# Optimization experiments

Measured on AMD Instinct MI355X. Metric: run time of the kernel, lower is better.

Reference implementation:

```python
import jax, jax.numpy as jnp
import numpy as np

B, N, K = 8, 2048, 32
EPS = 1e-5


def _lrelu(x):
    return jnp.where(x >= 0, x, 0.2 * x)


def _bn(x, p):
    # inference BatchNorm; x: [B, C, ...], p: [4, C] = (gamma, beta, mean, var)
    g, b, m, v = p[0], p[1], p[2], p[3]
    shape = (1, -1) + (1,) * (x.ndim - 2)
    scale = g * jax.lax.rsqrt(v + EPS)
    return (x - m.reshape(shape)) * scale.reshape(shape) + b.reshape(shape)


def _group(x, k):
    # ops.group with xyz_or_feature='feature', feature_or_diff='diff'
    # x: [B, C, N] -> edge features [B, 2C, N, k] = cat(neighbor - center, center)
    xt = jnp.transpose(x, (0, 2, 1))  # [B, N, C]
    sq = jnp.sum(xt * xt, axis=-1)    # [B, N]
    dist = sq[:, :, None] - 2.0 * jnp.einsum('bnc,bmc->bnm', xt, xt) + sq[:, None, :]
    idx = jax.lax.top_k(-dist, k)[1]  # [B, N, k] nearest neighbors
    nbr = jax.vmap(lambda f, i: f[i])(xt, idx)  # [B, N, k, C]
    center = xt[:, :, None, :]
    edge = jnp.concatenate([nbr - center, jnp.broadcast_to(center, nbr.shape)], axis=-1)
    return jnp.transpose(edge, (0, 3, 1, 2))  # [B, 2C, N, k]


def _edgeconv(x, w1, bn1, w2, bn2, k):
    e = _group(x, k)
    h = _lrelu(_bn(jnp.einsum('oc,bcnk->bonk', w1, e), bn1))
    h = _lrelu(_bn(jnp.einsum('oc,bcnk->bonk', w2, h), bn2))
    return jnp.max(h, axis=-1)  # max over neighbors -> [B, C_out, N]


def _model(x,
           ec1_w1, ec1_bn1, ec1_w2, ec1_bn2,
           ec2_w1, ec2_bn1, ec2_w2, ec2_bn2,
           ec3_w1, ec3_bn1, ec3_w2, ec3_bn2,
           emb_w, q_w, k_w, v_w, att_bn1, ff_w1, ff_w2, att_bn2,
           cb_w, cb_bn):
    # EdgeConvBlock (3 stacked EdgeConvs, outputs concatenated)
    f1 = _edgeconv(x, ec1_w1, ec1_bn1, ec1_w2, ec1_bn2, K)
    f2 = _edgeconv(f1, ec2_w1, ec2_bn1, ec2_w2, ec2_bn2, K)
    f3 = _edgeconv(f2, ec3_w1, ec3_bn1, ec3_w2, ec3_bn2, K)
    xc = jnp.concatenate([f1, f2, f3], axis=1)  # [B, 192, N]
    # Point2PointAttentionBlock: embedding then dense self-attention
    h = jnp.einsum('oc,bcn->bon', emb_w, xc)  # [B, 1024, N]
    q = jnp.einsum('oc,bcn->bon', q_w, h)
    kk = jnp.einsum('oc,bcn->bon', k_w, h)
    v = jnp.einsum('oc,bcn->bon', v_w, h)
    scale = jnp.sqrt(jnp.asarray(h.shape[1], h.dtype))
    att = jax.nn.softmax(jnp.einsum('bcn,bcm->bnm', q, kk) / scale, axis=-1)  # [B, N, N]
    x_r = jnp.einsum('bnm,bcm->bcn', att, v)
    h = _bn(h + x_r, att_bn1)
    ff = jnp.einsum('oc,bcn->bon', ff_w2, _lrelu(jnp.einsum('oc,bcn->bon', ff_w1, h)))
    h = _bn(h + ff, att_bn2)
    # ConvBlock head
    return _lrelu(_bn(jnp.einsum('oc,bcn->bon', cb_w, h), cb_bn))  # [B, 1024, N]


def setup_inputs() -> dict:
    key = jax.random.key(0)
    ks = iter(jax.random.split(key, 32))

    def randn(shape, s=0.1):
        return jax.random.normal(next(ks), shape, jnp.float32) * s

    def bnp(c):
        return jax.random.uniform(next(ks), (4, c), jnp.float32, 0.1, 1.0)

    return {
        'x': randn((B, 3, N), 1.0),
        'ec1_w1': randn((64, 6)), 'ec1_bn1': bnp(64),
        'ec1_w2': randn((64, 64)), 'ec1_bn2': bnp(64),
        'ec2_w1': randn((64, 128)), 'ec2_bn1': bnp(64),
        'ec2_w2': randn((64, 64)), 'ec2_bn2': bnp(64),
        'ec3_w1': randn((64, 128)), 'ec3_bn1': bnp(64),
        'ec3_w2': randn((64, 64)), 'ec3_bn2': bnp(64),
        'emb_w': randn((1024, 192), 0.05),
        'q_w': randn((1024, 1024), 0.03),
        'k_w': randn((1024, 1024), 0.03),
        'v_w': randn((1024, 1024), 0.03),
        'att_bn1': bnp(1024),
        'ff_w1': randn((512, 1024), 0.03),
        'ff_w2': randn((1024, 512), 0.03),
        'att_bn2': bnp(1024),
        'cb_w': randn((1024, 1024), 0.03),
        'cb_bn': bnp(1024),
    }


def reference(x,
              ec1_w1, ec1_bn1, ec1_w2, ec1_bn2,
              ec2_w1, ec2_bn1, ec2_w2, ec2_bn2,
              ec3_w1, ec3_bn1, ec3_w2, ec3_bn2,
              emb_w, q_w, k_w, v_w, att_bn1, ff_w1, ff_w2, att_bn2,
              cb_w, cb_bn):
    return _model(x,
                  ec1_w1, ec1_bn1, ec1_w2, ec1_bn2,
                  ec2_w1, ec2_bn1, ec2_w2, ec2_bn2,
                  ec3_w1, ec3_bn1, ec3_w2, ec3_bn2,
                  emb_w, q_w, k_w, v_w, att_bn1, ff_w1, ff_w2, att_bn2,
                  cb_w, cb_bn)
```

## Files before the change

### kernel.cpp

```cpp
#include <hip/hip_runtime.h>
#include <hip/hip_bf16.h>

constexpr int Bn  = 8;
constexpr int Np  = 2048;
constexpr int KNN = 32;

typedef __attribute__((ext_vector_type(8))) short bf16x8;
typedef __attribute__((ext_vector_type(4))) float f32x4;

__device__ static inline void gll16(const void* g, void* l) {
  __builtin_amdgcn_global_load_lds((const __attribute__((address_space(1))) void*)g,
                                   (__attribute__((address_space(3))) void*)l, 16, 0, 0);
}

__device__ static inline unsigned short f2bf(float x) {
  union { __hip_bfloat16 h; unsigned short u; } cv; cv.h = __float2bfloat16(x); return cv.u;
}
__device__ static inline float bf2f(unsigned short u) {
  union { __hip_bfloat16 h; unsigned short u; } cv; cv.u = u; return __bfloat162float(cv.h);
}

__global__ __launch_bounds__(256)
void cvt_bf16_kernel(const float* __restrict__ s, __hip_bfloat16* __restrict__ d, int n) {
  int i = blockIdx.x * 256 + threadIdx.x;
  if (i < n) d[i] = __float2bfloat16(s[i]);
}

template<int CIN, int K1>
__global__ __launch_bounds__(256)
void cvt_w1a(const float* __restrict__ w1, __hip_bfloat16* __restrict__ out) {
  int i = blockIdx.x * 256 + threadIdx.x;
  if (i >= 64 * K1) return;
  int o = i / K1, c = i - o * K1;
  out[i] = __float2bfloat16(c < CIN ? w1[o * 2 * CIN + c] : 0.f);
}

__global__ __launch_bounds__(256)
void xpose_kernel(const float* __restrict__ x, float* __restrict__ xt,
                  __hip_bfloat16* __restrict__ xb) {
  int i = blockIdx.x * 256 + threadIdx.x;
  int b = i >> 11, n = i & 2047;
  const float* p = x + (long)b * 3 * Np + n;
  float vx = p[0], vy = p[Np], vz = p[2 * Np];
  xt[(long)i * 4 + 0] = vx;
  xt[(long)i * 4 + 1] = vy;
  xt[(long)i * 4 + 2] = vz;
  xt[(long)i * 4 + 3] = 0.f;
  __hip_bfloat16* q = xb + (long)i * 8;
  q[0] = __float2bfloat16(vx); q[1] = __float2bfloat16(vy);
  q[2] = __float2bfloat16(vz);
  q[3] = __float2bfloat16(0.f); q[4] = q[3]; q[5] = q[3]; q[6] = q[3]; q[7] = q[3];
}

template<int C, int CP>
__global__ __launch_bounds__(256)
void sq_kernel(const float* __restrict__ f, float* __restrict__ out) {
  int i = blockIdx.x * 256 + threadIdx.x;
  const float* p = f + (long)i * CP;
  float s = 0.f;
#pragma unroll
  for (int c = 0; c < C; ++c) s += p[c] * p[c];
  out[i] = s;
}

__global__ __launch_bounds__(256)
void dist_kernel(const float* __restrict__ A, int lda, long sA,
                 float* __restrict__ C, long sC,
                 const float* __restrict__ sqB, int Kd) {
  int bz = blockIdx.z;
  A += (long)bz * sA;
  C += (long)bz * sC;
  sqB += (long)bz * Np;
  int i0 = blockIdx.y * 128, j0 = blockIdx.x * 128;
  __shared__ float As[8][128];
  __shared__ float Bs[8][128];
  float acc[8][8];
#pragma unroll
  for (int a = 0; a < 8; ++a)
#pragma unroll
    for (int b2 = 0; b2 < 8; ++b2) acc[a][b2] = 0.f;
  int t = threadIdx.x;
  int tx = t & 15, ty = t >> 4;
  for (int k0 = 0; k0 < Kd; k0 += 8) {
    {
      int ii = t >> 1, kk = (t & 1) * 4;
#pragma unroll
      for (int u = 0; u < 4; ++u) {
        int kg = k0 + kk + u;
        As[kk + u][ii] = (kg < Kd) ? A[(long)(i0 + ii) * lda + kg] : 0.f;
        Bs[kk + u][ii] = (kg < Kd) ? A[(long)(j0 + ii) * lda + kg] : 0.f;
      }
    }
    __syncthreads();
#pragma unroll
    for (int kk = 0; kk < 8; ++kk) {
      float av[8], bv[8];
#pragma unroll
      for (int u = 0; u < 8; ++u) av[u] = As[kk][ty * 8 + u];
#pragma unroll
      for (int u = 0; u < 8; ++u) bv[u] = Bs[kk][tx * 8 + u];
#pragma unroll
      for (int a = 0; a < 8; ++a)
#pragma unroll
        for (int b2 = 0; b2 < 8; ++b2) acc[a][b2] += av[a] * bv[b2];
    }
    __syncthreads();
  }
#pragma unroll
  for (int a = 0; a < 8; ++a) {
    int i = i0 + ty * 8 + a;
#pragma unroll
    for (int b2 = 0; b2 < 8; ++b2) {
      int j = j0 + tx * 8 + b2;
      C[(long)i * Np + j] = sqB[j] - 2.f * acc[a][b2];
    }
  }
}


__device__ static inline unsigned umin32(unsigned a, unsigned b) { return a < b ? a : b; }

__device__ static inline unsigned long long shfl64x(unsigned long long k, int m) {
  unsigned lo = (unsigned)__shfl_xor((int)(unsigned)k, m);
  unsigned hi = (unsigned)__shfl_xor((int)(unsigned)(k >> 32), m);
  return ((unsigned long long)hi << 32) | (unsigned long long)lo;
}

__device__ static inline unsigned lane_sort64_u32(unsigned v, int lane) {
#pragma unroll
  for (int k = 2; k <= 64; k <<= 1) {
#pragma unroll
    for (int j = k >> 1; j > 0; j >>= 1) {
      unsigned o = (unsigned)__shfl_xor((int)v, j);
      bool dir = ((lane & k) == 0);
      bool lower = ((lane & j) == 0);
      bool keep = (v < o) == (dir == lower);
      v = keep ? v : o;
    }
  }
  return v;
}

__device__ static inline unsigned long long lane_sort64_u64(unsigned long long v, int lane) {
#pragma unroll
  for (int k = 2; k <= 64; k <<= 1) {
#pragma unroll
    for (int j = k >> 1; j > 0; j >>= 1) {
      unsigned long long o = shfl64x(v, j);
      bool dir = ((lane & k) == 0);
      bool lower = ((lane & j) == 0);
      bool keep = (v < o) == (dir == lower);
      v = keep ? v : o;
    }
  }
  return v;
}

__device__ static inline unsigned long long lane_merge64(unsigned long long a,
                                                         unsigned long long b, int lane) {
  unsigned long long br = shfl64x(b, 63);
  unsigned long long m = a < br ? a : br;
#pragma unroll
  for (int j = 32; j > 0; j >>= 1) {
    unsigned long long o = shfl64x(m, j);
    bool lower = ((lane & j) == 0);
    bool keep = (m < o) == lower;
    m = keep ? m : o;
  }
  return m;
}

__global__ __launch_bounds__(64)
void topk_kernel(const float* __restrict__ D, int* __restrict__ idxOut) {
  long row = (long)blockIdx.y * Np + blockIdx.x;
  const float* rowp = D + row * Np;
  int lane = threadIdx.x;
  __shared__ unsigned long long buf[1024];

  unsigned val[32];
  const float4* rp = (const float4*)rowp;
#pragma unroll
  for (int j4 = 0; j4 < 8; ++j4) {
    float4 f4 = rp[j4 * 64 + lane];
    float fv[4] = {f4.x, f4.y, f4.z, f4.w};
#pragma unroll
    for (int u = 0; u < 4; ++u) {
      unsigned b = __float_as_uint(fv[u]);
      val[j4 * 4 + u] = b ^ ((unsigned)((int)b >> 31) | 0x80000000u);
    }
  }

  unsigned tmn[16];
#pragma unroll
  for (int i = 0; i < 16; ++i) tmn[i] = umin32(val[i], val[i + 16]);
#pragma unroll
  for (int w2 = 8; w2 >= 1; w2 >>= 1)
#pragma unroll
    for (int i = 0; i < 8; ++i)
      if (i < w2) tmn[i] = umin32(tmn[i], tmn[i + w2]);

  unsigned T = (unsigned)__shfl((int)lane_sort64_u32(tmn[0], lane), 31);

  int S = 0;
#pragma unroll
  for (int s = 0; s < 32; ++s) {
    bool p = val[s] <= T;
    unsigned long long mask = __ballot(p);
    int pre = __builtin_amdgcn_mbcnt_hi((unsigned)(mask >> 32),
              __builtin_amdgcn_mbcnt_lo((unsigned)mask, 0u));
    int pos = S + pre;
    if (p && pos < 1024) {
      unsigned idx = (unsigned)((s >> 2) * 256 + lane * 4 + (s & 3));
      buf[pos] = ((unsigned long long)val[s] << 32) | idx;
    }
    S += (int)__popcll(mask);
  }
  __syncthreads();

  unsigned long long cur;
  if (S <= 1024) {
    unsigned long long k0 = (lane < S) ? buf[lane] : ~0ull;
    cur = lane_sort64_u64(k0, lane);
    for (int c = 64; c < S; c += 64) {
      unsigned long long kc = (c + lane < S) ? buf[c + lane] : ~0ull;
      cur = lane_merge64(cur, lane_sort64_u64(kc, lane), lane);
    }
  } else {
    cur = ~0ull;
    for (int s = 0; s < 32; ++s) {
      unsigned idx = (unsigned)((s >> 2) * 256 + lane * 4 + (s & 3));
      unsigned long long kc = ((unsigned long long)val[s] << 32) | idx;
      cur = lane_merge64(cur, lane_sort64_u64(kc, lane), lane);
    }
  }
  if (lane < KNN) idxOut[row * KNN + lane] = (int)(unsigned)cur;
}

template<int CIN, int CP>
__global__ __launch_bounds__(256)
void biasker(const float* __restrict__ feat, const float* __restrict__ w1,
             float* __restrict__ bias) {
  __shared__ float wd[64][CIN + 1];
  int tid = threadIdx.x;
  for (int e = tid; e < 64 * CIN; e += 256) {
    int o = e / CIN, c = e - o * CIN;
    wd[o][c] = w1[o * 2 * CIN + CIN + c] - w1[o * 2 * CIN + c];
  }
  __syncthreads();
  int wv = tid >> 6, o = tid & 63;
  float wr_[CIN];
#pragma unroll
  for (int c = 0; c < CIN; ++c) wr_[c] = wd[o][c];
  long base = (long)blockIdx.y * Np + blockIdx.x * 32 + wv * 8;
  for (int p = 0; p < 8; ++p) {
    const float* fr = feat + (base + p) * CP;
    float acc = 0.f;
#pragma unroll
    for (int c = 0; c < CIN; ++c) acc = fmaf(wr_[c], fr[c], acc);
    bias[(base + p) * 64 + o] = acc;
  }
}

template<int K1>
__global__ __launch_bounds__(256)
void edge_mfma(const __hip_bfloat16* __restrict__ featb, int fstride,
               const int* __restrict__ idx, const float* __restrict__ bias,
               const __hip_bfloat16* __restrict__ w1b,
               const __hip_bfloat16* __restrict__ w2b,
               const float* __restrict__ bn1, const float* __restrict__ bn2,
               float* __restrict__ fout, __hip_bfloat16* __restrict__ xcseg) {
  __shared__ __align__(16) char lds[32768 + 64 * K1 * 2 + 8192 + 1024 + 512];
  __hip_bfloat16* A  = (__hip_bfloat16*)lds;
  __hip_bfloat16* H1 = A + 128 * K1;
  float*          H2 = (float*)lds;
  __hip_bfloat16* W1 = (__hip_bfloat16*)(lds + 32768);
  __hip_bfloat16* W2 = W1 + 64 * K1;
  float* biasS = (float*)(lds + 32768 + 64 * K1 * 2 + 8192);
  int*   idxS  = (int*)(biasS + 256);

  int t = threadIdx.x, lane = t & 63, w = t >> 6;
  long pb = (long)blockIdx.y * Np;
  int p0 = blockIdx.x * 4;

  if (t < 128) idxS[t] = idx[(pb + p0 + (t >> 5)) * KNN + (t & 31)];
  biasS[w * 64 + lane] = bias[(pb + p0 + w) * 64 + lane];
  for (int e = t; e < 64 * K1 / 8; e += 256)
    ((ulonglong2*)W1)[e] = ((const ulonglong2*)w1b)[e];
  for (int e = t; e < 512; e += 256)
    ((ulonglong2*)W2)[e] = ((const ulonglong2*)w2b)[e];
  __syncthreads();

  if (K1 == 64) {
#pragma unroll
    for (int i = 0; i < 4; ++i) {
      int e = t + i * 256;
      int r = e >> 3, cc = e & 7;
      const ulonglong2* src = (const ulonglong2*)(featb + (pb + idxS[r]) * fstride) + cc;
      ((ulonglong2*)(A + r * 64))[cc] = *src;
    }
  } else {
    if (t < 128) {
      int r = t;
      ulonglong2 z; z.x = 0; z.y = 0;
      ((ulonglong2*)(A + r * 32))[0] = *(const ulonglong2*)(featb + (pb + idxS[r]) * fstride);
      ((ulonglong2*)(A + r * 32))[1] = z;
      ((ulonglong2*)(A + r * 32))[2] = z;
      ((ulonglong2*)(A + r * 32))[3] = z;
    }
  }

  int ocol = lane & 15;
  float sc1[4], sh1[4], sc2[4], sh2[4];
#pragma unroll
  for (int jn = 0; jn < 4; ++jn) {
    int o = jn * 16 + ocol;
    sc1[jn] = bn1[o] * rsqrtf(bn1[192 + o] + 1e-5f);
    sh1[jn] = bn1[64 + o] - bn1[128 + o] * sc1[jn];
    sc2[jn] = bn2[o] * rsqrtf(bn2[192 + o] + 1e-5f);
    sh2[jn] = bn2[64 + o] - bn2[128 + o] * sc2[jn];
  }
  __syncthreads();

  int mrow = lane & 15;
  int kc   = (lane >> 4) * 8;
  constexpr int KS = K1 / 32;

  f32x4 acc[2][4];
#pragma unroll
  for (int im = 0; im < 2; ++im)
#pragma unroll
    for (int jn = 0; jn < 4; ++jn) acc[im][jn] = f32x4{0.f, 0.f, 0.f, 0.f};
#pragma unroll
  for (int s = 0; s < KS; ++s) {
    bf16x8 af[2], bf_[4];
#pragma unroll
    for (int im = 0; im < 2; ++im)
      af[im] = *(const bf16x8*)(A + (w * 32 + im * 16 + mrow) * K1 + s * 32 + kc);
#pragma unroll
    for (int jn = 0; jn < 4; ++jn)
      bf_[jn] = *(const bf16x8*)(W1 + (jn * 16 + mrow) * K1 + s * 32 + kc);
#pragma unroll
    for (int im = 0; im < 2; ++im)
#pragma unroll
      for (int jn = 0; jn < 4; ++jn)
        acc[im][jn] = __builtin_amdgcn_mfma_f32_16x16x32_bf16(af[im], bf_[jn], acc[im][jn], 0, 0, 0);
  }
#pragma unroll
  for (int im = 0; im < 2; ++im)
#pragma unroll
    for (int jn = 0; jn < 4; ++jn) {
      int o = jn * 16 + ocol;
      float bsv = biasS[w * 64 + o];
#pragma unroll
      for (int r = 0; r < 4; ++r) {
        int m = w * 32 + im * 16 + (lane >> 4) * 4 + r;
        float x = (acc[im][jn][r] + bsv) * sc1[jn] + sh1[jn];
        x = fmaxf(x, 0.2f * x);
        H1[m * 64 + o] = __float2bfloat16(x);
      }
    }
  __syncthreads();

  bf16x8 a2[2][2], b2[4][2];
#pragma unroll
  for (int im = 0; im < 2; ++im)
#pragma unroll
    for (int s = 0; s < 2; ++s)
      a2[im][s] = *(const bf16x8*)(H1 + (w * 32 + im * 16 + mrow) * 64 + s * 32 + kc);
#pragma unroll
  for (int jn = 0; jn < 4; ++jn)
#pragma unroll
    for (int s = 0; s < 2; ++s)
      b2[jn][s] = *(const bf16x8*)(W2 + (jn * 16 + mrow) * 64 + s * 32 + kc);
  __syncthreads();

  f32x4 acc2[2][4];
#pragma unroll
  for (int im = 0; im < 2; ++im)
#pragma unroll
    for (int jn = 0; jn < 4; ++jn) acc2[im][jn] = f32x4{0.f, 0.f, 0.f, 0.f};
#pragma unroll
  for (int s = 0; s < 2; ++s)
#pragma unroll
    for (int im = 0; im < 2; ++im)
#pragma unroll
      for (int jn = 0; jn < 4; ++jn)
        acc2[im][jn] = __builtin_amdgcn_mfma_f32_16x16x32_bf16(a2[im][s], b2[jn][s], acc2[im][jn], 0, 0, 0);
#pragma unroll
  for (int im = 0; im < 2; ++im)
#pragma unroll
    for (int jn = 0; jn < 4; ++jn) {
      int o = jn * 16 + ocol;
#pragma unroll
      for (int r = 0; r < 4; ++r) {
        int m = w * 32 + im * 16 + (lane >> 4) * 4 + r;
        float x = acc2[im][jn][r] * sc2[jn] + sh2[jn];
        x = fmaxf(x, 0.2f * x);
        H2[m * 64 + o] = x;
      }
    }
  __syncthreads();

  {
    int o = t & 63;
    float m = -3.4e38f;
#pragma unroll
    for (int k = 0; k < 32; ++k) m = fmaxf(m, H2[(w * 32 + k) * 64 + o]);
    int n2 = p0 + w;
    if (fout) fout[(pb + n2) * 64 + o] = m;
    xcseg[(pb + n2) * 192 + o] = __float2bfloat16(m);
  }
}

template<int OUTF, int BNMODE, int RESID, int LRELU>
__global__ __launch_bounds__(256)
void gemm_tn(const __hip_bfloat16* __restrict__ A, int lda, long sA,
             const __hip_bfloat16* __restrict__ B, int ldb, long sB,
             void* __restrict__ Cv, int ldc, long sC,
             const __hip_bfloat16* __restrict__ R, long sR,
             const float* __restrict__ bn, int bnlen, int Kd) {
  int bz = blockIdx.z;
  A += (long)bz * sA;
  B += (long)bz * sB;
  __shared__ __hip_bfloat16 As[128 * 32];
  __shared__ __hip_bfloat16 Bs[128 * 32];
  int t = threadIdx.x, lane = t & 63, w = t >> 6;
  int wm = w & 1, wn = w >> 1;
  long i0 = (long)blockIdx.x * 128, j0 = (long)blockIdx.y * 128;
  f32x4 acc[4][4];
#pragma unroll
  for (int i = 0; i < 4; ++i)
#pragma unroll
    for (int j = 0; j < 4; ++j) acc[i][j] = f32x4{0.f, 0.f, 0.f, 0.f};

  int srow = w * 16 + (lane >> 2);
  int sch  = (lane & 3) * 8;
  const __hip_bfloat16* ga0 = A + (i0 + srow) * lda + sch;
  const __hip_bfloat16* ga1 = A + (i0 + 64 + srow) * lda + sch;
  const __hip_bfloat16* gb0 = B + (j0 + srow) * ldb + sch;
  const __hip_bfloat16* gb1 = B + (j0 + 64 + srow) * ldb + sch;
  __hip_bfloat16* la0 = As + (w * 16) * 32;
  __hip_bfloat16* la1 = As + (64 + w * 16) * 32;
  __hip_bfloat16* lb0 = Bs + (w * 16) * 32;
  __hip_bfloat16* lb1 = Bs + (64 + w * 16) * 32;
  const __hip_bfloat16* pa = As + (wm * 64 + (lane & 15)) * 32 + (lane >> 4) * 8;
  const __hip_bfloat16* pb = Bs + (wn * 64 + (lane & 15)) * 32 + (lane >> 4) * 8;

  for (int k0 = 0; k0 < Kd; k0 += 32) {
    gll16(ga0, la0);
    gll16(ga1, la1);
    gll16(gb0, lb0);
    gll16(gb1, lb1);
    ga0 += 32; ga1 += 32; gb0 += 32; gb1 += 32;
    __syncthreads();
    bf16x8 af[4], bfv[4];
#pragma unroll
    for (int i = 0; i < 4; ++i) af[i]  = *(const bf16x8*)(pa + i * 16 * 32);
#pragma unroll
    for (int j = 0; j < 4; ++j) bfv[j] = *(const bf16x8*)(pb + j * 16 * 32);
#pragma unroll
    for (int i = 0; i < 4; ++i)
#pragma unroll
      for (int j = 0; j < 4; ++j)
        acc[i][j] = __builtin_amdgcn_mfma_f32_16x16x32_bf16(af[i], bfv[j], acc[i][j], 0, 0, 0);
    __syncthreads();
  }

  int mlocal = (lane >> 4) * 4;
  int nlocal = lane & 15;
#pragma unroll
  for (int i = 0; i < 4; ++i) {
    long m0 = i0 + wm * 64 + i * 16 + mlocal;
    float bsc[4], bsh[4];
    if (BNMODE == 1) {
#pragma unroll
      for (int r = 0; r < 4; ++r) {
        long c = m0 + r;
        float sc = bn[c] * rsqrtf(bn[3 * bnlen + c] + 1e-5f);
        bsc[r] = sc;
        bsh[r] = bn[bnlen + c] - bn[2 * bnlen + c] * sc;
      }
    }
#pragma unroll
    for (int j = 0; j < 4; ++j) {
      long nn = j0 + wn * 64 + j * 16 + nlocal;
      float sc2 = 1.f, sh2 = 0.f;
      if (BNMODE == 2) {
        sc2 = bn[nn] * rsqrtf(bn[3 * bnlen + nn] + 1e-5f);
        sh2 = bn[bnlen + nn] - bn[2 * bnlen + nn] * sc2;
      }
      f32x4 v = acc[i][j];
      float o4[4];
      ushort4 rv;
      if (RESID) rv = *(const ushort4*)(R + (long)bz * sR + nn * ldc + m0);
#pragma unroll
      for (int r = 0; r < 4; ++r) {
        float x = v[r];
        if (RESID) x += bf2f(r == 0 ? rv.x : r == 1 ? rv.y : r == 2 ? rv.z : rv.w);
        if (BNMODE == 1) x = x * bsc[r] + bsh[r];
        if (BNMODE == 2) x = x * sc2 + sh2;
        if (LRELU) x = (x >= 0.f) ? x : 0.2f * x;
        o4[r] = x;
      }
      if (OUTF) {
        float* Cp = (float*)Cv + (long)bz * sC + nn * ldc + m0;
        *(float4*)Cp = make_float4(o4[0], o4[1], o4[2], o4[3]);
      } else {
        __hip_bfloat16* Cp = (__hip_bfloat16*)Cv + (long)bz * sC + nn * ldc + m0;
        ushort4 sv;
        sv.x = f2bf(o4[0]); sv.y = f2bf(o4[1]); sv.z = f2bf(o4[2]); sv.w = f2bf(o4[3]);
        *(ushort4*)Cp = sv;
      }
    }
  }
}

__global__ __launch_bounds__(256)
void softmax_bf(__hip_bfloat16* __restrict__ S) {
  long row = (long)blockIdx.y * Np + blockIdx.x;
  __hip_bfloat16* p = S + row * Np;
  int t = threadIdx.x;
  const float scale = 0.03125f;
  float v[8];
  float mx = -3.4e38f;
#pragma unroll
  for (int u = 0; u < 8; ++u) {
    v[u] = __bfloat162float(p[u * 256 + t]) * scale;
    mx = fmaxf(mx, v[u]);
  }
  __shared__ float red[4];
#pragma unroll
  for (int off = 32; off > 0; off >>= 1) mx = fmaxf(mx, __shfl_xor(mx, off));
  if ((t & 63) == 0) red[t >> 6] = mx;
  __syncthreads();
  mx = fmaxf(fmaxf(red[0], red[1]), fmaxf(red[2], red[3]));
  __syncthreads();
  float sum = 0.f;
#pragma unroll
  for (int u = 0; u < 8; ++u) { v[u] = __expf(v[u] - mx); sum += v[u]; }
#pragma unroll
  for (int off = 32; off > 0; off >>= 1) sum += __shfl_xor(sum, off);
  if ((t & 63) == 0) red[t >> 6] = sum;
  __syncthreads();
  sum = red[0] + red[1] + red[2] + red[3];
  float inv = 1.f / sum;
#pragma unroll
  for (int u = 0; u < 8; ++u) p[u * 256 + t] = __float2bfloat16(v[u] * inv);
}

extern "C" void kernel_launch(void* const* d_in, const int* in_sizes, int n_in,
                              void* d_out, int out_size, void* d_ws, size_t ws_size,
                              hipStream_t stream) {
  const float* x       = (const float*)d_in[0];
  const float* ec1_w1  = (const float*)d_in[1];
  const float* ec1_bn1 = (const float*)d_in[2];
  const float* ec1_w2  = (const float*)d_in[3];
  const float* ec1_bn2 = (const float*)d_in[4];
  const float* ec2_w1  = (const float*)d_in[5];
  const float* ec2_bn1 = (const float*)d_in[6];
  const float* ec2_w2  = (const float*)d_in[7];
  const float* ec2_bn2 = (const float*)d_in[8];
  const float* ec3_w1  = (const float*)d_in[9];
  const float* ec3_bn1 = (const float*)d_in[10];
  const float* ec3_w2  = (const float*)d_in[11];
  const float* ec3_bn2 = (const float*)d_in[12];
  const float* emb_w   = (const float*)d_in[13];
  const float* q_w     = (const float*)d_in[14];
  const float* k_w     = (const float*)d_in[15];
  const float* v_w     = (const float*)d_in[16];
  const float* att_bn1 = (const float*)d_in[17];
  const float* ff_w1   = (const float*)d_in[18];
  const float* ff_w2   = (const float*)d_in[19];
  const float* att_bn2 = (const float*)d_in[20];
  const float* cb_w    = (const float*)d_in[21];
  const float* cb_bn   = (const float*)d_in[22];
  float* out = (float*)d_out;
  (void)in_sizes; (void)n_in; (void)out_size; (void)ws_size;

  float* ws  = (float*)d_ws;
  float* xt  = ws;
  float* f1  = xt + 65536;
  float* f2  = f1 + 1048576;
  float* sqb = f2 + 1048576;
  int*   idxb = (int*)(sqb + 16384);
  __hip_bfloat16* xc  = (__hip_bfloat16*)(idxb + 524288);
  __hip_bfloat16* wts = xc + 3145728;
  __hip_bfloat16* ew  = wts + 5439488;
  __hip_bfloat16* xb  = ew + 22528;
  float* big = (float*)(xb + 131072);
  __hip_bfloat16* hb  = (__hip_bfloat16*)big;
  __hip_bfloat16* qb  = hb + 16777216;
  __hip_bfloat16* kb  = qb + 16777216;
  __hip_bfloat16* vtb = kb + 16777216;
  __hip_bfloat16* Sb  = vtb + 16777216;
  float* dist = big;
  float* biasb = big + 33554432;

  __hip_bfloat16* emb_wb = wts;
  __hip_bfloat16* q_wb   = wts + 196608;
  __hip_bfloat16* k_wb   = wts + 1245184;
  __hip_bfloat16* v_wb   = wts + 2293760;
  __hip_bfloat16* ff1_wb = wts + 3342336;
  __hip_bfloat16* ff2_wb = wts + 3866624;
  __hip_bfloat16* cb_wb  = wts + 4390912;

  __hip_bfloat16* w1a1_b = ew;
  __hip_bfloat16* w2_1b  = ew + 2048;
  __hip_bfloat16* w1a2_b = ew + 6144;
  __hip_bfloat16* w2_2b  = ew + 10240;
  __hip_bfloat16* w1a3_b = ew + 14336;
  __hip_bfloat16* w2_3b  = ew + 18432;

  const long sN1024 = (long)Np * 1024;
  const long sN512  = (long)Np * 512;
  const long sN192  = (long)Np * 192;
  const long sNN    = (long)Np * Np;

  cvt_bf16_kernel<<<768,  256, 0, stream>>>(emb_w, emb_wb, 196608);
  cvt_bf16_kernel<<<4096, 256, 0, stream>>>(q_w,   q_wb,   1048576);
  cvt_bf16_kernel<<<4096, 256, 0, stream>>>(k_w,   k_wb,   1048576);
  cvt_bf16_kernel<<<4096, 256, 0, stream>>>(v_w,   v_wb,   1048576);
  cvt_bf16_kernel<<<2048, 256, 0, stream>>>(ff_w1, ff1_wb, 524288);
  cvt_bf16_kernel<<<2048, 256, 0, stream>>>(ff_w2, ff2_wb, 524288);
  cvt_bf16_kernel<<<4096, 256, 0, stream>>>(cb_w,  cb_wb,  1048576);
  cvt_w1a<3, 32><<<8, 256, 0, stream>>>(ec1_w1, w1a1_b);
  cvt_w1a<64, 64><<<16, 256, 0, stream>>>(ec2_w1, w1a2_b);
  cvt_w1a<64, 64><<<16, 256, 0, stream>>>(ec3_w1, w1a3_b);
  cvt_bf16_kernel<<<16, 256, 0, stream>>>(ec1_w2, w2_1b, 4096);
  cvt_bf16_kernel<<<16, 256, 0, stream>>>(ec2_w2, w2_2b, 4096);
  cvt_bf16_kernel<<<16, 256, 0, stream>>>(ec3_w2, w2_3b, 4096);

  xpose_kernel<<<64, 256, 0, stream>>>(x, xt, xb);

  sq_kernel<3, 4><<<64, 256, 0, stream>>>(xt, sqb);
  dist_kernel<<<dim3(16, 16, Bn), 256, 0, stream>>>(xt, 4, (long)Np * 4, dist, sNN, sqb, 3);
  topk_kernel<<<dim3(Np, Bn), 64, 0, stream>>>(dist, idxb);
  biasker<3, 4><<<dim3(Np / 32, Bn), 256, 0, stream>>>(xt, ec1_w1, biasb);
  edge_mfma<32><<<dim3(Np / 4, Bn), 256, 0, stream>>>(
      xb, 8, idxb, biasb, w1a1_b, w2_1b, ec1_bn1, ec1_bn2, f1, xc);

  sq_kernel<64, 64><<<64, 256, 0, stream>>>(f1, sqb);
  dist_kernel<<<dim3(16, 16, Bn), 256, 0, stream>>>(f1, 64, (long)Np * 64, dist, sNN, sqb, 64);
  topk_kernel<<<dim3(Np, Bn), 64, 0, stream>>>(dist, idxb);
  biasker<64, 64><<<dim3(Np / 32, Bn), 256, 0, stream>>>(f1, ec2_w1, biasb);
  edge_mfma<64><<<dim3(Np / 4, Bn), 256, 0, stream>>>(
      xc, 192, idxb, biasb, w1a2_b, w2_2b, ec2_bn1, ec2_bn2, f2, xc + 64);

  sq_kernel<64, 64><<<64, 256, 0, stream>>>(f2, sqb);
  dist_kernel<<<dim3(16, 16, Bn), 256, 0, stream>>>(f2, 64, (long)Np * 64, dist, sNN, sqb, 64);
  topk_kernel<<<dim3(Np, Bn), 64, 0, stream>>>(dist, idxb);
  biasker<64, 64><<<dim3(Np / 32, Bn), 256, 0, stream>>>(f2, ec3_w1, biasb);
  edge_mfma<64><<<dim3(Np / 4, Bn), 256, 0, stream>>>(
      xc + 64, 192, idxb, biasb, w1a3_b, w2_3b, ec3_bn1, ec3_bn2, nullptr, xc + 128);

  gemm_tn<0, 0, 0, 0><<<dim3(8, 16, Bn), 256, 0, stream>>>(
      emb_wb, 192, 0, xc, 192, sN192, hb, 1024, sN1024, nullptr, 0, nullptr, 0, 192);

  gemm_tn<0, 0, 0, 0><<<dim3(8, 16, Bn), 256, 0, stream>>>(
      q_wb, 1024, 0, hb, 1024, sN1024, qb, 1024, sN1024, nullptr, 0, nullptr, 0, 1024);
  gemm_tn<0, 0, 0, 0><<<dim3(8, 16, Bn), 256, 0, stream>>>(
      k_wb, 1024, 0, hb, 1024, sN1024, kb, 1024, sN1024, nullptr, 0, nullptr, 0, 1024);
  gemm_tn<0, 0, 0, 0><<<dim3(16, 8, Bn), 256, 0, stream>>>(
      hb, 1024, sN1024, v_wb, 1024, 0, vtb, 2048, sN1024, nullptr, 0, nullptr, 0, 1024);

  gemm_tn<0, 0, 0, 0><<<dim3(16, 16, Bn), 256, 0, stream>>>(
      kb, 1024, sN1024, qb, 1024, sN1024, Sb, 2048, sNN, nullptr, 0, nullptr, 0, 1024);
  softmax_bf<<<dim3(Np, Bn), 256, 0, stream>>>(Sb);

  gemm_tn<0, 1, 1, 0><<<dim3(8, 16, Bn), 256, 0, stream>>>(
      vtb, 2048, sN1024, Sb, 2048, sNN, hb, 1024, sN1024, hb, sN1024, att_bn1, 1024, 2048);

  gemm_tn<0, 0, 0, 1><<<dim3(4, 16, Bn), 256, 0, stream>>>(
      ff1_wb, 1024, 0, hb, 1024, sN1024, qb, 512, sN512, nullptr, 0, nullptr, 0, 1024);
  gemm_tn<0, 1, 1, 0><<<dim3(8, 16, Bn), 256, 0, stream>>>(
      ff2_wb, 512, 0, qb, 512, sN512, hb, 1024, sN1024, hb, sN1024, att_bn2, 1024, 512);

  gemm_tn<1, 2, 0, 1><<<dim3(16, 8, Bn), 256, 0, stream>>>(
      hb, 1024, sN1024, cb_wb, 1024, 0, out, 2048, sN1024, nullptr, 0, cb_bn, 1024, 1024);
}
```

Baseline: 1.145 ms.

## Add double-buffered 256x256 tile GEMM with XCD-aware block remapping for attention GEMMs

Introduces a new gemm_db kernel with 256x256 output tiles, 512 threads and eight waves. It double-buffers K-tiles in LDS via async global-to-LDS loads using an XOR swizzle, and remaps the flat block index so neighbouring tiles land on the same XCD. Most large GEMMs (QKV, scores, attention-value, ff2, final conv) now use it instead of the 128x128 gemm_tn. The goal is more operand reuse per tile and overlap of loads with MFMA compute. In exchange it uses a large LDS footprint (128KB) and many accumulator registers, which cuts occupancy and leaves fewer workgroups per launch.

Result: faster. 979.0 us (-14.5%).

```diff
diff --git a/kernel.cpp b/kernel.cpp
--- a/kernel.cpp
+++ b/kernel.cpp
@@ -471,6 +471,142 @@
 #pragma unroll
   for (int i = 0; i < 4; ++i) {
     long m0 = i0 + wm * 64 + i * 16 + mlocal;
+    float bsc[4], bsh[4];
+    if (BNMODE == 1) {
+#pragma unroll
+      for (int r = 0; r < 4; ++r) {
+        long c = m0 + r;
+        float sc = bn[c] * rsqrtf(bn[3 * bnlen + c] + 1e-5f);
+        bsc[r] = sc;
+        bsh[r] = bn[bnlen + c] - bn[2 * bnlen + c] * sc;
+      }
+    }
+#pragma unroll
+    for (int j = 0; j < 4; ++j) {
+      long nn = j0 + wn * 64 + j * 16 + nlocal;
+      float sc2 = 1.f, sh2 = 0.f;
+      if (BNMODE == 2) {
+        sc2 = bn[nn] * rsqrtf(bn[3 * bnlen + nn] + 1e-5f);
+        sh2 = bn[bnlen + nn] - bn[2 * bnlen + nn] * sc2;
+      }
+      f32x4 v = acc[i][j];
+      float o4[4];
+      ushort4 rv;
+      if (RESID) rv = *(const ushort4*)(R + (long)bz * sR + nn * ldc + m0);
+#pragma unroll
+      for (int r = 0; r < 4; ++r) {
+        float x = v[r];
+        if (RESID) x += bf2f(r == 0 ? rv.x : r == 1 ? rv.y : r == 2 ? rv.z : rv.w);
+        if (BNMODE == 1) x = x * bsc[r] + bsh[r];
+        if (BNMODE == 2) x = x * sc2 + sh2;
+        if (LRELU) x = (x >= 0.f) ? x : 0.2f * x;
+        o4[r] = x;
+      }
+      if (OUTF) {
+        float* Cp = (float*)Cv + (long)bz * sC + nn * ldc + m0;
+        *(float4*)Cp = make_float4(o4[0], o4[1], o4[2], o4[3]);
+      } else {
+        __hip_bfloat16* Cp = (__hip_bfloat16*)Cv + (long)bz * sC + nn * ldc + m0;
+        ushort4 sv;
+        sv.x = f2bf(o4[0]); sv.y = f2bf(o4[1]); sv.z = f2bf(o4[2]); sv.w = f2bf(o4[3]);
+        *(ushort4*)Cp = sv;
+      }
+    }
+  }
+}
+
+template<int OUTF, int BNMODE, int RESID, int LRELU>
+__global__ __launch_bounds__(512)
+void gemm_db(const __hip_bfloat16* __restrict__ A, int lda, long sA,
+             const __hip_bfloat16* __restrict__ B, int ldb, long sB,
+             void* __restrict__ Cv, int ldc, long sC,
+             const __hip_bfloat16* __restrict__ R, long sR,
+             const float* __restrict__ bn, int bnlen, int Kd,
+             int gx, int gy) {
+  int nwg = gx * gy * Bn;
+  int cpx = nwg >> 3;
+  int orig = blockIdx.x;
+  int wg = (orig & 7) * cpx + (orig >> 3);
+  int bz = wg / (gx * gy);
+  int rem = wg - bz * (gx * gy);
+  int by = rem / gx;
+  int bx = rem - by * gx;
+  A += (long)bz * sA;
+  B += (long)bz * sB;
+  long i0 = (long)bx * 256, j0 = (long)by * 256;
+
+  __shared__ __hip_bfloat16 As[2][256 * 64];
+  __shared__ __hip_bfloat16 Bs[2][256 * 64];
+
+  int t = threadIdx.x, lane = t & 63, w = t >> 6;
+  int wm = w & 1, wn = w >> 1;
+
+  f32x4 acc[8][4];
+#pragma unroll
+  for (int im = 0; im < 8; ++im)
+#pragma unroll
+    for (int jn = 0; jn < 4; ++jn) acc[im][jn] = f32x4{0.f, 0.f, 0.f, 0.f};
+
+#define STAGE_DB(bi, kt)                                                     \
+  {                                                                          \
+    _Pragma("unroll")                                                        \
+    for (int i = 0; i < 4; ++i) {                                            \
+      int e = t + i * 512;                                                   \
+      int r = e >> 3, c = e & 7;                                             \
+      int cs = c ^ (r & 7);                                                  \
+      gll16(A + (i0 + r) * lda + (kt) * 64 + cs * 8,                         \
+            (__hip_bfloat16*)As[bi] + e * 8);                                \
+    }                                                                        \
+    _Pragma("unroll")                                                        \
+    for (int i = 0; i < 4; ++i) {                                            \
+      int e = t + i * 512;                                                   \
+      int r = e >> 3, c = e & 7;                                             \
+      int cs = c ^ (r & 7);                                                  \
+      gll16(B + (j0 + r) * ldb + (kt) * 64 + cs * 8,                         \
+            (__hip_bfloat16*)Bs[bi] + e * 8);                                \
+    }                                                                        \
+  }
+
+  int nt = Kd >> 6;
+  STAGE_DB(0, 0);
+  __syncthreads();
+
+  int cur = 0;
+  for (int kt = 0; kt < nt; ++kt) {
+    if (kt + 1 < nt) STAGE_DB(cur ^ 1, kt + 1);
+    const __hip_bfloat16* Ab = As[cur];
+    const __hip_bfloat16* Bb = Bs[cur];
+#pragma unroll
+    for (int ks = 0; ks < 2; ++ks) {
+      bf16x8 af[8], bfv[4];
+#pragma unroll
+      for (int im = 0; im < 8; ++im) {
+        int ra = wm * 128 + im * 16 + (lane & 15);
+        int q = (ks * 4 + (lane >> 4)) ^ (ra & 7);
+        af[im] = *(const bf16x8*)(Ab + ra * 64 + q * 8);
+      }
+#pragma unroll
+      for (int jn = 0; jn < 4; ++jn) {
+        int rb = wn * 64 + jn * 16 + (lane & 15);
+        int q = (ks * 4 + (lane >> 4)) ^ (rb & 7);
+        bfv[jn] = *(const bf16x8*)(Bb + rb * 64 + q * 8);
+      }
+#pragma unroll
+      for (int im = 0; im < 8; ++im)
+#pragma unroll
+        for (int jn = 0; jn < 4; ++jn)
+          acc[im][jn] = __builtin_amdgcn_mfma_f32_16x16x32_bf16(af[im], bfv[jn], acc[im][jn], 0, 0, 0);
+    }
+    __syncthreads();
+    cur ^= 1;
+  }
+#undef STAGE_DB
+
+  int mlocal = (lane >> 4) * 4;
+  int nlocal = lane & 15;
+#pragma unroll
+  for (int i = 0; i < 8; ++i) {
+    long m0 = i0 + wm * 128 + i * 16 + mlocal;
     float bsc[4], bsh[4];
     if (BNMODE == 1) {
 #pragma unroll
@@ -656,25 +792,25 @@
   gemm_tn<0, 0, 0, 0><<<dim3(8, 16, Bn), 256, 0, stream>>>(
       emb_wb, 192, 0, xc, 192, sN192, hb, 1024, sN1024, nullptr, 0, nullptr, 0, 192);
 
-  gemm_tn<0, 0, 0, 0><<<dim3(8, 16, Bn), 256, 0, stream>>>(
-      q_wb, 1024, 0, hb, 1024, sN1024, qb, 1024, sN1024, nullptr, 0, nullptr, 0, 1024);
-  gemm_tn<0, 0, 0, 0><<<dim3(8, 16, Bn), 256, 0, stream>>>(
-      k_wb, 1024, 0, hb, 1024, sN1024, kb, 1024, sN1024, nullptr, 0, nullptr, 0, 1024);
-  gemm_tn<0, 0, 0, 0><<<dim3(16, 8, Bn), 256, 0, stream>>>(
-      hb, 1024, sN1024, v_wb, 1024, 0, vtb, 2048, sN1024, nullptr, 0, nullptr, 0, 1024);
-
-  gemm_tn<0, 0, 0, 0><<<dim3(16, 16, Bn), 256, 0, stream>>>(
-      kb, 1024, sN1024, qb, 1024, sN1024, Sb, 2048, sNN, nullptr, 0, nullptr, 0, 1024);
+  gemm_db<0, 0, 0, 0><<<dim3(4 * 8 * Bn), 512, 0, stream>>>(
+      q_wb, 1024, 0, hb, 1024, sN1024, qb, 1024, sN1024, nullptr, 0, nullptr, 0, 1024, 4, 8);
+  gemm_db<0, 0, 0, 0><<<dim3(4 * 8 * Bn), 512, 0, stream>>>(
+      k_wb, 1024, 0, hb, 1024, sN1024, kb, 1024, sN1024, nullptr, 0, nullptr, 0, 1024, 4, 8);
+  gemm_db<0, 0, 0, 0><<<dim3(8 * 4 * Bn), 512, 0, stream>>>(
+      hb, 1024, sN1024, v_wb, 1024, 0, vtb, 2048, sN1024, nullptr, 0, nullptr, 0, 1024, 8, 4);
+
+  gemm_db<0, 0, 0, 0><<<dim3(8 * 8 * Bn), 512, 0, stream>>>(
+      kb, 1024, sN1024, qb, 1024, sN1024, Sb, 2048, sNN, nullptr, 0, nullptr, 0, 1024, 8, 8);
   softmax_bf<<<dim3(Np, Bn), 256, 0, stream>>>(Sb);
 
-  gemm_tn<0, 1, 1, 0><<<dim3(8, 16, Bn), 256, 0, stream>>>(
-      vtb, 2048, sN1024, Sb, 2048, sNN, hb, 1024, sN1024, hb, sN1024, att_bn1, 1024, 2048);
+  gemm_db<0, 1, 1, 0><<<dim3(4 * 8 * Bn), 512, 0, stream>>>(
+      vtb, 2048, sN1024, Sb, 2048, sNN, hb, 1024, sN1024, hb, sN1024, att_bn1, 1024, 2048, 4, 8);
 
   gemm_tn<0, 0, 0, 1><<<dim3(4, 16, Bn), 256, 0, stream>>>(
       ff1_wb, 1024, 0, hb, 1024, sN1024, qb, 512, sN512, nullptr, 0, nullptr, 0, 1024);
-  gemm_tn<0, 1, 1, 0><<<dim3(8, 16, Bn), 256, 0, stream>>>(
-      ff2_wb, 512, 0, qb, 512, sN512, hb, 1024, sN1024, hb, sN1024, att_bn2, 1024, 512);
-
-  gemm_tn<1, 2, 0, 1><<<dim3(16, 8, Bn), 256, 0, stream>>>(
-      hb, 1024, sN1024, cb_wb, 1024, 0, out, 2048, sN1024, nullptr, 0, cb_bn, 1024, 1024);
-}
+  gemm_db<0, 1, 1, 0><<<dim3(4 * 8 * Bn), 512, 0, stream>>>(
+      ff2_wb, 512, 0, qb, 512, sN512, hb, 1024, sN1024, hb, sN1024, att_bn2, 1024, 512, 4, 8);
+
+  gemm_db<1, 2, 0, 1><<<dim3(8 * 4 * Bn), 512, 0, stream>>>(
+      hb, 1024, sN1024, cb_wb, 1024, 0, out, 2048, sN1024, nullptr, 0, cb_bn, 1024, 1024, 8, 4);
+}
```
